# Performance work log

Hardware: AMD Instinct MI355X
Metric: run time of the kernel (lower is better)

## Reference

```python
import jax, jax.numpy as jnp
import numpy as np

N_NODES = 100000
N_EDGES = 1600000
D_IN = 128
D_HID = 128
D_OUT = 128


def setup_inputs() -> dict:
    key = jax.random.key(0)
    ks = jax.random.split(key, 8)
    x = jax.random.normal(ks[0], (N_NODES, D_IN), dtype=jnp.float32)
    edge_index = jax.random.randint(ks[1], (2, N_EDGES), 0, N_NODES, dtype=jnp.int64)
    s = 1.0 / np.sqrt(D_IN)
    W1 = jax.random.normal(ks[2], (D_IN, D_HID), dtype=jnp.float32) * s
    W2 = jax.random.normal(ks[3], (D_HID, D_HID), dtype=jnp.float32) * s
    W3 = jax.random.normal(ks[4], (D_HID, D_OUT), dtype=jnp.float32) * s
    b1 = jnp.zeros((D_HID,), jnp.float32)
    b2 = jnp.zeros((D_HID,), jnp.float32)
    b3 = jnp.zeros((D_OUT,), jnp.float32)
    return {"x": x, "edge_index": edge_index, "W1": W1, "b1": b1,
            "W2": W2, "b2": b2, "W3": W3, "b3": b3}


def reference(x, edge_index, W1, b1, W2, b2, W3, b3):
    # PyG GCNConv semantics: add self-loops, symmetric deg^{-1/2} normalization,
    # message = norm * (x W)[src], scatter-add into dst, then + bias; ReLU after each layer.
    n = x.shape[0]
    loops = jnp.arange(n, dtype=edge_index.dtype)
    src = jnp.concatenate([edge_index[0], loops])  # [E+N]
    dst = jnp.concatenate([edge_index[1], loops])  # [E+N]
    deg = jax.ops.segment_sum(jnp.ones_like(dst, dtype=x.dtype), dst, num_segments=n)
    dinv = jnp.where(deg > 0, jax.lax.rsqrt(deg), 0.0)
    norm = (dinv[src] * dinv[dst])[:, None]  # [E+N, 1]

    def layer(h, W, b):
        h = h @ W                                     # [N, d_out] small GEMM
        msg = h[src] * norm                           # gather + scale  [E+N, d_out]
        agg = jax.ops.segment_sum(msg, dst, num_segments=n)  # scatter-add
        return jax.nn.relu(agg + b)

    x = layer(x, W1, b1)
    x = layer(x, W2, b2)
    x = layer(x, W3, b3)
    return x
```

## Files before the change

kernel.cpp:

```cpp
#include <hip/hip_runtime.h>

#define NN 100000
#define NE 1600000
#define DD 128
#define NB 98
#define NGRP 8
#define NPG (NN / NGRP)
#define CSRCAP 1900032
#define NBLK_B 1024
#define EPB 1563
#define BCAP 210000
#define WJ 256
#define NW 49
#define NSUB (NGRP * NW)
#define SCAP 4608
#define LCAP 5632

typedef __attribute__((ext_vector_type(8))) short short8;
typedef __attribute__((ext_vector_type(4))) float f32x4;

__device__ __forceinline__ unsigned bf16rn(float f) {
  unsigned u = __float_as_uint(f);
  return (u + 0x7fffu + ((u >> 16) & 1u)) >> 16;
}
__device__ __forceinline__ unsigned pk2(float a, float b) {
  return bf16rn(a) | (bf16rn(b) << 16);
}
__device__ __forceinline__ float lo_f(unsigned u) { return __uint_as_float(u << 16); }
__device__ __forceinline__ float hi_f(unsigned u) { return __uint_as_float(u & 0xffff0000u); }


__global__ __launch_bounds__(256) void k_init(int* __restrict__ cnt,
                                              int* __restrict__ gcur,
                                              int* __restrict__ scur) {
  int i = blockIdx.x * 256 + threadIdx.x;
  if (i < NN) cnt[i] = 0;
  if (i < NGRP) gcur[i] = 0;
  if (i < NSUB) scur[i] = 0;
}

__global__ __launch_bounds__(256) void k_bucket(const void* __restrict__ ei,
                                                int* __restrict__ bsrc,
                                                int* __restrict__ bdst,
                                                int* __restrict__ gcur) {
  __shared__ int lcnt[NGRP], lbase[NGRP], lcur[NGRP], zcnt;
  const int t = threadIdx.x;
  if (t == 0) zcnt = 0;
  if (t < NGRP) { lcnt[t] = 0; lcur[t] = 0; }
  __syncthreads();
  if (t < 64) {
    const unsigned* w = (const unsigned*)ei;
    int z = 0;
    for (int i = t; i < 256; i += 64)
      if (w[2 * i + 1] == 0u) z++;
    atomicAdd(&zcnt, z);
  }
  __syncthreads();
  const int isLL = (zcnt >= 250);
  const long long e0 = (long long)blockIdx.x * EPB;
  const int nE = (int)((NE - e0) < EPB ? (NE - e0) : EPB);
  int es[7], ed[7], eb[7];
#pragma unroll
  for (int k = 0; k < 7; k++) {
    int idx = t + k * 256;
    eb[k] = -1;
    if (idx < nE) {
      long long e = e0 + idx;
      if (isLL) {
        es[k] = (int)((const long long*)ei)[e];
        ed[k] = (int)((const long long*)ei)[NE + e];
      } else {
        es[k] = ((const int*)ei)[e];
        ed[k] = ((const int*)ei)[NE + e];
      }
      eb[k] = ed[k] / NPG;
      atomicAdd(&lcnt[eb[k]], 1);
    }
  }
  __syncthreads();
  if (t < NGRP) lbase[t] = atomicAdd(&gcur[t], lcnt[t]);
  __syncthreads();
#pragma unroll
  for (int k = 0; k < 7; k++) {
    if (eb[k] >= 0) {
      int p = lbase[eb[k]] + atomicAdd(&lcur[eb[k]], 1);
      size_t o = (size_t)eb[k] * BCAP + p;
      bsrc[o] = es[k];
      bdst[o] = ed[k];
    }
  }
}

__global__ __launch_bounds__(256) void k_sub(const int* __restrict__ bsrc,
                                             const int* __restrict__ bdst,
                                             const int* __restrict__ gcur,
                                             int* __restrict__ cnt,
                                             int* __restrict__ ssrc,
                                             int* __restrict__ sdst,
                                             int* __restrict__ scur) {
  __shared__ int lcnt[NW], lbase[NW], lcur[NW];
  const int g = blockIdx.x & (NGRP - 1);
  const int s = blockIdx.x >> 3;
  const int n = gcur[g];
  const int chunk = (n + 15) >> 4;
  const int e0 = s * chunk;
  const int e1 = min(e0 + chunk, n);
  const int t = threadIdx.x;
  if (t < NW) { lcnt[t] = 0; lcur[t] = 0; }
  __syncthreads();
  const int* dp = bdst + (size_t)g * BCAP;
  const int* sp = bsrc + (size_t)g * BCAP;
  for (int i = e0 + t; i < e1; i += 256) {
    int d = dp[i];
    atomicAdd(&cnt[d], 1);
    atomicAdd(&lcnt[(d - g * NPG) >> 8], 1);
  }
  __syncthreads();
  if (t < NW) lbase[t] = atomicAdd(&scur[g * NW + t], lcnt[t]);
  __syncthreads();
  for (int i = e0 + t; i < e1; i += 256) {
    int d = dp[i];
    int srcv = sp[i];
    int w = (d - g * NPG) >> 8;
    int p = lbase[w] + atomicAdd(&lcur[w], 1);
    size_t o = (size_t)(g * NW + w) * SCAP + p;
    ssrc[o] = srcv;
    sdst[o] = d;
  }
}

__global__ __launch_bounds__(256) void k_dinv(const int* __restrict__ cnt,
                                              float* __restrict__ dinv) {
  int i = blockIdx.x * 256 + threadIdx.x;
  if (i < NN) dinv[i] = rsqrtf((float)(cnt[i] + 1));
}

__global__ __launch_bounds__(256) void k_scan1(const int* __restrict__ cnt,
                                               int* __restrict__ bsums) {
  __shared__ int sd[256];
  const int tid = threadIdx.x;
  const int base = blockIdx.x * 1024;
  int s = 0;
#pragma unroll
  for (int j = 0; j < 4; j++) {
    int i = base + tid * 4 + j;
    if (i < NN) s += (cnt[i] + 3) & ~3;
  }
  sd[tid] = s;
  __syncthreads();
  for (int d = 128; d > 0; d >>= 1) {
    if (tid < d) sd[tid] += sd[tid + d];
    __syncthreads();
  }
  if (tid == 0) bsums[blockIdx.x] = sd[0];
}

__global__ __launch_bounds__(128) void k_scan2(int* __restrict__ bsums,
                                               int* __restrict__ offs) {
  __shared__ int sd[128];
  const int tid = threadIdx.x;
  int v = (tid < NB) ? bsums[tid] : 0;
  sd[tid] = v;
  __syncthreads();
  for (int d = 1; d < 128; d <<= 1) {
    int t = (tid >= d) ? sd[tid - d] : 0;
    __syncthreads();
    sd[tid] += t;
    __syncthreads();
  }
  if (tid < NB) bsums[tid] = sd[tid] - v;
  if (tid == 127) offs[NN] = sd[127];
}

__global__ __launch_bounds__(256) void k_scan3(const int* __restrict__ cnt,
                                               const int* __restrict__ bsums,
                                               int* __restrict__ offs) {
  __shared__ int sd[256];
  const int tid = threadIdx.x;
  const int base = blockIdx.x * 1024;
  int v[4];
  int s = 0;
#pragma unroll
  for (int j = 0; j < 4; j++) {
    int i = base + tid * 4 + j;
    v[j] = (i < NN) ? ((cnt[i] + 3) & ~3) : 0;
    s += v[j];
  }
  sd[tid] = s;
  __syncthreads();
  for (int d = 1; d < 256; d <<= 1) {
    int t = (tid >= d) ? sd[tid - d] : 0;
    __syncthreads();
    if (tid >= d) sd[tid] += t;
    __syncthreads();
  }
  int run = bsums[blockIdx.x] + sd[tid] - s;
#pragma unroll
  for (int j = 0; j < 4; j++) {
    int i = base + tid * 4 + j;
    if (i < NN) offs[i] = run;
    run += v[j];
  }
}

__global__ __launch_bounds__(256) void k_csr(const int* __restrict__ ssrc,
                                             const int* __restrict__ sdst,
                                             const int* __restrict__ scur,
                                             const int* __restrict__ offs,
                                             int* __restrict__ csr) {
  __shared__ int L[LCAP];
  __shared__ int loff[WJ], lcur[WJ];
  __shared__ int sR0, sRlen, sm;
  const int b = blockIdx.x;
  const int g = b / NW, w = b % NW;
  const int n0 = g * NPG + w * WJ;
  const int wn = min(WJ, NPG - w * WJ);
  const int t = threadIdx.x;
  for (int i = t; i < LCAP; i += 256) L[i] = NN;
  if (t == 0) {
    sR0 = offs[n0];
    sRlen = offs[n0 + wn] - sR0;
    sm = scur[b];
  }
  __syncthreads();
  const int R0 = sR0, Rlen = sRlen, m = sm;
  for (int i = t; i < wn; i += 256) {
    loff[i] = offs[n0 + i] - R0;
    lcur[i] = 0;
  }
  __syncthreads();
  const int* sp = ssrc + (size_t)b * SCAP;
  const int* dp = sdst + (size_t)b * SCAP;
  for (int e = t; e < m; e += 256) {
    int dl = dp[e] - n0;
    int pos = loff[dl] + atomicAdd(&lcur[dl], 1);
    if (pos < LCAP) L[pos] = sp[e];
  }
  __syncthreads();
  for (int i = t * 4; i < Rlen; i += 1024)
    if (i + 3 < LCAP) *(int4*)(csr + R0 + i) = *(const int4*)&L[i];
}

__global__ __launch_bounds__(256) void k_prepw(const float* __restrict__ Wa,
                                               const float* __restrict__ Wb,
                                               const float* __restrict__ Wc,
                                               unsigned* __restrict__ wt,
                                               unsigned* __restrict__ tbuf) {
  if (blockIdx.x == 0 && threadIdx.x < 64)
    tbuf[(size_t)NN * 64 + threadIdx.x] = 0u;
  int id = blockIdx.x * 256 + threadIdx.x;
  int layer = id >> 13;
  int r = id & 8191;
  int n = r >> 6, kp = r & 63;
  const float* W = (layer == 0) ? Wa : (layer == 1) ? Wb : Wc;
  wt[(size_t)layer * 8192 + n * 64 + kp] =
      pk2(W[(size_t)(2 * kp) * DD + n], W[(size_t)(2 * kp + 1) * DD + n]);
}

template <bool F32SRC>
__global__ __launch_bounds__(256) void k_gemm(const void* __restrict__ Av,
                                              const unsigned* __restrict__ Wg,
                                              const float* __restrict__ dinv,
                                              unsigned* __restrict__ T) {
  __shared__ char lds[49408];
  const int t = threadIdx.x;
  const int row0 = blockIdx.x * 64;
  const int w = t >> 6, l = t & 63;
  const int lm = l & 15, kb = l >> 4;

  {
    int r = t >> 2;
    int gr = row0 + r;
#pragma unroll
    for (int s4 = 0; s4 < 4; s4++) {
      int sg = (t & 3) * 4 + s4;
      uint4 u;
      if (gr < NN) {
        if (F32SRC) {
          const float* ap = (const float*)Av + (size_t)gr * DD + sg * 8;
          float4 f0 = *(const float4*)ap;
          float4 f1 = *(const float4*)(ap + 4);
          u.x = pk2(f0.x, f0.y); u.y = pk2(f0.z, f0.w);
          u.z = pk2(f1.x, f1.y); u.w = pk2(f1.z, f1.w);
        } else {
          u = *(const uint4*)((const unsigned*)Av + (size_t)gr * 64 + sg * 4);
        }
      } else {
        u = make_uint4(0u, 0u, 0u, 0u);
      }
      *(uint4*)(lds + r * 256 + ((sg * 16) ^ ((r & 7) << 4))) = u;
    }
  }
#pragma unroll
  for (int q = 0; q < 8; q++) {
    int e = t * 8 + q;
    int n = e >> 4, sg = e & 15;
    uint4 u = *(const uint4*)(Wg + n * 64 + sg * 4);
    *(uint4*)(lds + 16384 + n * 256 + ((sg * 16) ^ ((n & 7) << 4))) = u;
  }
  if (t < 64) {
    int gr = row0 + t;
    *(float*)(lds + 49152 + t * 4) = (gr < NN) ? dinv[gr] : 0.f;
  }
  __syncthreads();

  f32x4 acc[4][2];
#pragma unroll
  for (int i = 0; i < 4; i++)
#pragma unroll
    for (int j = 0; j < 2; j++) acc[i][j] = (f32x4){0.f, 0.f, 0.f, 0.f};

#pragma unroll
  for (int kk = 0; kk < 4; kk++) {
    const int koff = (kk * 4 + kb) * 16;
    short8 af[4], bf[2];
#pragma unroll
    for (int i = 0; i < 4; i++) {
      int r = i * 16 + lm;
      af[i] = *(const short8*)(lds + r * 256 + (koff ^ ((r & 7) << 4)));
    }
#pragma unroll
    for (int j = 0; j < 2; j++) {
      int n = w * 32 + j * 16 + lm;
      bf[j] = *(const short8*)(lds + 16384 + n * 256 + (koff ^ ((n & 7) << 4)));
    }
#pragma unroll
    for (int i = 0; i < 4; i++)
#pragma unroll
      for (int j = 0; j < 2; j++)
        acc[i][j] = __builtin_amdgcn_mfma_f32_16x16x32_bf16(af[i], bf[j], acc[i][j], 0, 0, 0);
  }

#pragma unroll
  for (int i = 0; i < 4; i++) {
#pragma unroll
    for (int j = 0; j < 2; j++) {
#pragma unroll
      for (int q = 0; q < 4; q++) {
        int rl = i * 16 + (l >> 4) * 4 + q;
        float s = *(const float*)(lds + 49152 + rl * 4);
        float v = acc[i][j][q] * s;
        float nb = __shfl_xor(v, 1);
        if ((l & 1) == 0) {
          int gr = row0 + rl;
          if (gr < NN) {
            int cp = w * 16 + j * 8 + (lm >> 1);
            T[(size_t)gr * 64 + cp] = pk2(v, nb);
          }
        }
      }
    }
  }
}

template <bool BF16OUT>
__global__ __launch_bounds__(256) void k_agg(const unsigned* __restrict__ T,
                                             const int* __restrict__ offs,
                                             const int* __restrict__ csr,
                                             const float* __restrict__ dinv,
                                             const float* __restrict__ bias,
                                             void* __restrict__ outv) {
  const int lane = threadIdx.x & 63;
  const int node = blockIdx.x * 4 + (threadIdx.x >> 6);
  if (node >= NN) return;
  unsigned su = T[(size_t)node * 64 + lane];
  float accx = lo_f(su), accy = hi_f(su);
  int j = offs[node];
  const int end = offs[node + 1];
  for (; j + 16 <= end; j += 16) {
    int4 c0 = *(const int4*)(csr + j);
    int4 c1 = *(const int4*)(csr + j + 4);
    int4 c2 = *(const int4*)(csr + j + 8);
    int4 c3 = *(const int4*)(csr + j + 12);
    unsigned u0 = T[(size_t)c0.x * 64 + lane];
    unsigned u1 = T[(size_t)c0.y * 64 + lane];
    unsigned u2 = T[(size_t)c0.z * 64 + lane];
    unsigned u3 = T[(size_t)c0.w * 64 + lane];
    unsigned u4 = T[(size_t)c1.x * 64 + lane];
    unsigned u5 = T[(size_t)c1.y * 64 + lane];
    unsigned u6 = T[(size_t)c1.z * 64 + lane];
    unsigned u7 = T[(size_t)c1.w * 64 + lane];
    unsigned u8 = T[(size_t)c2.x * 64 + lane];
    unsigned u9 = T[(size_t)c2.y * 64 + lane];
    unsigned ua = T[(size_t)c2.z * 64 + lane];
    unsigned ub = T[(size_t)c2.w * 64 + lane];
    unsigned uc = T[(size_t)c3.x * 64 + lane];
    unsigned ud = T[(size_t)c3.y * 64 + lane];
    unsigned ue = T[(size_t)c3.z * 64 + lane];
    unsigned uf = T[(size_t)c3.w * 64 + lane];
    accx += (((lo_f(u0) + lo_f(u1)) + (lo_f(u2) + lo_f(u3))) +
             ((lo_f(u4) + lo_f(u5)) + (lo_f(u6) + lo_f(u7)))) +
            (((lo_f(u8) + lo_f(u9)) + (lo_f(ua) + lo_f(ub))) +
             ((lo_f(uc) + lo_f(ud)) + (lo_f(ue) + lo_f(uf))));
    accy += (((hi_f(u0) + hi_f(u1)) + (hi_f(u2) + hi_f(u3))) +
             ((hi_f(u4) + hi_f(u5)) + (hi_f(u6) + hi_f(u7)))) +
            (((hi_f(u8) + hi_f(u9)) + (hi_f(ua) + hi_f(ub))) +
             ((hi_f(uc) + hi_f(ud)) + (hi_f(ue) + hi_f(uf))));
  }
  for (; j < end; j += 4) {
    int4 c = *(const int4*)(csr + j);
    unsigned u0 = T[(size_t)c.x * 64 + lane];
    unsigned u1 = T[(size_t)c.y * 64 + lane];
    unsigned u2 = T[(size_t)c.z * 64 + lane];
    unsigned u3 = T[(size_t)c.w * 64 + lane];
    accx += (lo_f(u0) + lo_f(u1)) + (lo_f(u2) + lo_f(u3));
    accy += (hi_f(u0) + hi_f(u1)) + (hi_f(u2) + hi_f(u3));
  }
  float s = dinv[node];
  float2 bb = ((const float2*)bias)[lane];
  float ox = fmaxf(accx * s + bb.x, 0.f);
  float oy = fmaxf(accy * s + bb.y, 0.f);
  if (BF16OUT)
    ((unsigned*)outv)[(size_t)node * 64 + lane] = pk2(ox, oy);
  else
    ((float2*)outv)[(size_t)node * 64 + lane] = make_float2(ox, oy);
}


extern "C" void kernel_launch(void* const* d_in, const int* in_sizes, int n_in,
                              void* d_out, int out_size, void* d_ws, size_t ws_size,
                              hipStream_t stream) {
  const float* x = (const float*)d_in[0];
  const void* ei = (const void*)d_in[1];
  const float* W1 = (const float*)d_in[2];
  const float* b1 = (const float*)d_in[3];
  const float* W2 = (const float*)d_in[4];
  const float* b2 = (const float*)d_in[5];
  const float* W3 = (const float*)d_in[6];
  const float* b3 = (const float*)d_in[7];
  float* out = (float*)d_out;

  char* p = (char*)d_ws;
  auto take = [&](size_t bytes) {
    char* r = p;
    p += (bytes + 1023) & ~(size_t)1023;
    return r;
  };
  int* flagpad = (int*)take(4);  (void)flagpad;
  int* gcur = (int*)take((size_t)NGRP * 4);
  int* scur = (int*)take((size_t)NSUB * 4);
  int* cnt = (int*)take((size_t)NN * 4);
  int* offs = (int*)take((size_t)(NN + 1) * 4);
  int* bsums = (int*)take((size_t)NB * 4);
  float* dinv = (float*)take((size_t)NN * 4);
  unsigned* wt = (unsigned*)take((size_t)3 * DD * 64 * 4);
  int* csr = (int*)take((size_t)CSRCAP * 4);
  char* regA = (char*)take((size_t)(NN + 1) * 64 * 4);
  unsigned* tbuf = (unsigned*)regA;
  int* ssrc = (int*)regA;
  int* sdst = ssrc + (size_t)NSUB * SCAP;
  char* regB = (char*)take((size_t)NN * 64 * 4);
  unsigned* hbuf = (unsigned*)regB;
  int* bsrc = (int*)regB;
  int* bdst = bsrc + (size_t)NGRP * BCAP;

  const int nb_n = (NN + 255) / 256;

  k_init<<<nb_n, 256, 0, stream>>>(cnt, gcur, scur);
  k_bucket<<<NBLK_B, 256, 0, stream>>>(ei, bsrc, bdst, gcur);
  k_sub<<<128, 256, 0, stream>>>(bsrc, bdst, gcur, cnt, ssrc, sdst, scur);
  k_dinv<<<nb_n, 256, 0, stream>>>(cnt, dinv);
  k_scan1<<<NB, 256, 0, stream>>>(cnt, bsums);
  k_scan2<<<1, 128, 0, stream>>>(bsums, offs);
  k_scan3<<<NB, 256, 0, stream>>>(cnt, bsums, offs);
  k_csr<<<NSUB, 256, 0, stream>>>(ssrc, sdst, scur, offs, csr);
  k_prepw<<<96, 256, 0, stream>>>(W1, W2, W3, wt, tbuf);

  const int gb = (NN + 63) / 64;
  const int ab = (NN + 3) / 4;
  k_gemm<true><<<gb, 256, 0, stream>>>(x, wt, dinv, tbuf);
  k_agg<true><<<ab, 256, 0, stream>>>(tbuf, offs, csr, dinv, b1, hbuf);
  k_gemm<false><<<gb, 256, 0, stream>>>(hbuf, wt + 8192, dinv, tbuf);
  k_agg<true><<<ab, 256, 0, stream>>>(tbuf, offs, csr, dinv, b2, hbuf);
  k_gemm<false><<<gb, 256, 0, stream>>>(hbuf, wt + 16384, dinv, tbuf);
  k_agg<false><<<ab, 256, 0, stream>>>(tbuf, offs, csr, dinv, b3, out);
}
```

Measured before the change: 486.4 us.

## Pack edge src and local dst into one word and count degrees per window

```diff
diff --git a/kernel.cpp b/kernel.cpp
--- a/kernel.cpp
+++ b/kernel.cpp
@@ -15,6 +15,8 @@
 #define NSUB (NGRP * NW)
 #define SCAP 4608
 #define LCAP 5632
+#define NSLOT 64
+
 
 typedef __attribute__((ext_vector_type(8))) short short8;
 typedef __attribute__((ext_vector_type(4))) float f32x4;
@@ -30,23 +32,22 @@
 __device__ __forceinline__ float hi_f(unsigned u) { return __uint_as_float(u & 0xffff0000u); }
 
 
-__global__ __launch_bounds__(256) void k_init(int* __restrict__ cnt,
-                                              int* __restrict__ gcur,
+__global__ __launch_bounds__(256) void k_init(int* __restrict__ gcur,
                                               int* __restrict__ scur) {
   int i = blockIdx.x * 256 + threadIdx.x;
-  if (i < NN) cnt[i] = 0;
   if (i < NGRP) gcur[i] = 0;
   if (i < NSUB) scur[i] = 0;
 }
 
 __global__ __launch_bounds__(256) void k_bucket(const void* __restrict__ ei,
-                                                int* __restrict__ bsrc,
-                                                int* __restrict__ bdst,
+                                                int* __restrict__ bpk,
                                                 int* __restrict__ gcur) {
-  __shared__ int lcnt[NGRP], lbase[NGRP], lcur[NGRP], zcnt;
+  __shared__ int lcnt[4][NGRP], wbase[4][NGRP], lcur[4][NGRP];
+  __shared__ int zcnt;
   const int t = threadIdx.x;
+  const int wv = t >> 6;
   if (t == 0) zcnt = 0;
-  if (t < NGRP) { lcnt[t] = 0; lcur[t] = 0; }
+  if (t < 4 * NGRP) { ((int*)lcnt)[t] = 0; ((int*)lcur)[t] = 0; }
   __syncthreads();
   if (t < 64) {
     const unsigned* w = (const unsigned*)ei;
@@ -59,74 +60,99 @@
   const int isLL = (zcnt >= 250);
   const long long e0 = (long long)blockIdx.x * EPB;
   const int nE = (int)((NE - e0) < EPB ? (NE - e0) : EPB);
-  int es[7], ed[7], eb[7];
+  int epk[7], eb[7];
 #pragma unroll
   for (int k = 0; k < 7; k++) {
     int idx = t + k * 256;
     eb[k] = -1;
     if (idx < nE) {
       long long e = e0 + idx;
+      int s, d;
       if (isLL) {
-        es[k] = (int)((const long long*)ei)[e];
-        ed[k] = (int)((const long long*)ei)[NE + e];
+        s = (int)((const long long*)ei)[e];
+        d = (int)((const long long*)ei)[NE + e];
       } else {
-        es[k] = ((const int*)ei)[e];
-        ed[k] = ((const int*)ei)[NE + e];
+        s = ((const int*)ei)[e];
+        d = ((const int*)ei)[NE + e];
       }
-      eb[k] = ed[k] / NPG;
-      atomicAdd(&lcnt[eb[k]], 1);
+      int b = d / NPG;
+      eb[k] = b;
+      epk[k] = s | ((d - b * NPG) << 17);
+      atomicAdd(&lcnt[wv][b], 1);
     }
   }
   __syncthreads();
-  if (t < NGRP) lbase[t] = atomicAdd(&gcur[t], lcnt[t]);
+  if (t < NGRP) {
+    int c0 = lcnt[0][t], c1 = lcnt[1][t], c2 = lcnt[2][t], c3 = lcnt[3][t];
+    int base = atomicAdd(&gcur[t], c0 + c1 + c2 + c3);
+    wbase[0][t] = base;
+    wbase[1][t] = base + c0;
+    wbase[2][t] = base + c0 + c1;
+    wbase[3][t] = base + c0 + c1 + c2;
+  }
   __syncthreads();
 #pragma unroll
   for (int k = 0; k < 7; k++) {
     if (eb[k] >= 0) {
-      int p = lbase[eb[k]] + atomicAdd(&lcur[eb[k]], 1);
-      size_t o = (size_t)eb[k] * BCAP + p;
-      bsrc[o] = es[k];
-      bdst[o] = ed[k];
+      int p = wbase[wv][eb[k]] + atomicAdd(&lcur[wv][eb[k]], 1);
+      bpk[(size_t)eb[k] * BCAP + p] = epk[k];
     }
   }
 }
 
-__global__ __launch_bounds__(256) void k_sub(const int* __restrict__ bsrc,
-                                             const int* __restrict__ bdst,
+__global__ __launch_bounds__(256) void k_sub(const int* __restrict__ bpk,
                                              const int* __restrict__ gcur,
-                                             int* __restrict__ cnt,
-                                             int* __restrict__ ssrc,
-                                             int* __restrict__ sdst,
+                                             int* __restrict__ ssub,
                                              int* __restrict__ scur) {
-  __shared__ int lcnt[NW], lbase[NW], lcur[NW];
+  __shared__ int lcnt[4][NW], wbase[4][NW], lcur[4][NW];
   const int g = blockIdx.x & (NGRP - 1);
   const int s = blockIdx.x >> 3;
   const int n = gcur[g];
-  const int chunk = (n + 15) >> 4;
+  const int chunk = (n + NSLOT - 1) / NSLOT;
   const int e0 = s * chunk;
   const int e1 = min(e0 + chunk, n);
   const int t = threadIdx.x;
-  if (t < NW) { lcnt[t] = 0; lcur[t] = 0; }
-  __syncthreads();
-  const int* dp = bdst + (size_t)g * BCAP;
-  const int* sp = bsrc + (size_t)g * BCAP;
+  const int wv = t >> 6;
+  for (int i = t; i < 4 * NW; i += 256) { ((int*)lcnt)[i] = 0; ((int*)lcur)[i] = 0; }
+  __syncthreads();
+  const int* pb = bpk + (size_t)g * BCAP;
+  for (int i = e0 + t; i < e1; i += 256)
+    atomicAdd(&lcnt[wv][pb[i] >> 25], 1);
+  __syncthreads();
+  if (t < NW) {
+    int c0 = lcnt[0][t], c1 = lcnt[1][t], c2 = lcnt[2][t], c3 = lcnt[3][t];
+    int base = atomicAdd(&scur[g * NW + t], c0 + c1 + c2 + c3);
+    wbase[0][t] = base;
+    wbase[1][t] = base + c0;
+    wbase[2][t] = base + c0 + c1;
+    wbase[3][t] = base + c0 + c1 + c2;
+  }
+  __syncthreads();
   for (int i = e0 + t; i < e1; i += 256) {
-    int d = dp[i];
-    atomicAdd(&cnt[d], 1);
-    atomicAdd(&lcnt[(d - g * NPG) >> 8], 1);
-  }
-  __syncthreads();
-  if (t < NW) lbase[t] = atomicAdd(&scur[g * NW + t], lcnt[t]);
-  __syncthreads();
-  for (int i = e0 + t; i < e1; i += 256) {
-    int d = dp[i];
-    int srcv = sp[i];
-    int w = (d - g * NPG) >> 8;
-    int p = lbase[w] + atomicAdd(&lcur[w], 1);
-    size_t o = (size_t)(g * NW + w) * SCAP + p;
-    ssrc[o] = srcv;
-    sdst[o] = d;
-  }
+    int pk = pb[i];
+    int w = pk >> 25;
+    int p = wbase[wv][w] + atomicAdd(&lcur[wv][w], 1);
+    ssub[(size_t)(g * NW + w) * SCAP + p] = pk;
+  }
+}
+
+__global__ __launch_bounds__(256) void k_cnt(const int* __restrict__ ssub,
+                                             const int* __restrict__ scur,
+                                             int* __restrict__ cnt) {
+  __shared__ int lc[WJ];
+  const int b = blockIdx.x;
+  const int g = b / NW, w = b % NW;
+  const int n0 = g * NPG + w * WJ;
+  const int wn = min(WJ, NPG - w * WJ);
+  const int t = threadIdx.x;
+  lc[t] = 0;
+  __syncthreads();
+  const int m = scur[b];
+  const int* sp = ssub + (size_t)b * SCAP;
+  for (int e = t; e < m; e += 256)
+    atomicAdd(&lc[(sp[e] >> 17) & 255], 1);
+  __syncthreads();
+  if (t < wn) cnt[n0 + t] = lc[t];
 }
 
 __global__ __launch_bounds__(256) void k_dinv(const int* __restrict__ cnt,
@@ -203,8 +229,7 @@
   }
 }
 
-__global__ __launch_bounds__(256) void k_csr(const int* __restrict__ ssrc,
-                                             const int* __restrict__ sdst,
+__global__ __launch_bounds__(256) void k_csr(const int* __restrict__ ssub,
                                              const int* __restrict__ scur,
                                              const int* __restrict__ offs,
                                              int* __restrict__ csr) {
@@ -229,12 +254,12 @@
     lcur[i] = 0;
   }
   __syncthreads();
-  const int* sp = ssrc + (size_t)b * SCAP;
-  const int* dp = sdst + (size_t)b * SCAP;
+  const int* sp = ssub + (size_t)b * SCAP;
   for (int e = t; e < m; e += 256) {
-    int dl = dp[e] - n0;
+    int pk = sp[e];
+    int dl = (pk >> 17) & 255;
     int pos = loff[dl] + atomicAdd(&lcur[dl], 1);
-    if (pos < LCAP) L[pos] = sp[e];
+    if (pos < LCAP) L[pos] = pk & 0x1FFFF;
   }
   __syncthreads();
   for (int i = t * 4; i < Rlen; i += 1024)
@@ -436,7 +461,6 @@
     p += (bytes + 1023) & ~(size_t)1023;
     return r;
   };
-  int* flagpad = (int*)take(4);  (void)flagpad;
   int* gcur = (int*)take((size_t)NGRP * 4);
   int* scur = (int*)take((size_t)NSUB * 4);
   int* cnt = (int*)take((size_t)NN * 4);
@@ -447,23 +471,22 @@
   int* csr = (int*)take((size_t)CSRCAP * 4);
   char* regA = (char*)take((size_t)(NN + 1) * 64 * 4);
   unsigned* tbuf = (unsigned*)regA;
-  int* ssrc = (int*)regA;
-  int* sdst = ssrc + (size_t)NSUB * SCAP;
+  int* ssub = (int*)regA;
   char* regB = (char*)take((size_t)NN * 64 * 4);
   unsigned* hbuf = (unsigned*)regB;
-  int* bsrc = (int*)regB;
-  int* bdst = bsrc + (size_t)NGRP * BCAP;
+  int* bpk = (int*)regB;
 
   const int nb_n = (NN + 255) / 256;
 
-  k_init<<<nb_n, 256, 0, stream>>>(cnt, gcur, scur);
-  k_bucket<<<NBLK_B, 256, 0, stream>>>(ei, bsrc, bdst, gcur);
-  k_sub<<<128, 256, 0, stream>>>(bsrc, bdst, gcur, cnt, ssrc, sdst, scur);
+  k_init<<<2, 256, 0, stream>>>(gcur, scur);
+  k_bucket<<<NBLK_B, 256, 0, stream>>>(ei, bpk, gcur);
+  k_sub<<<NGRP * NSLOT, 256, 0, stream>>>(bpk, gcur, ssub, scur);
+  k_cnt<<<NSUB, 256, 0, stream>>>(ssub, scur, cnt);
   k_dinv<<<nb_n, 256, 0, stream>>>(cnt, dinv);
   k_scan1<<<NB, 256, 0, stream>>>(cnt, bsums);
   k_scan2<<<1, 128, 0, stream>>>(bsums, offs);
   k_scan3<<<NB, 256, 0, stream>>>(cnt, bsums, offs);
-  k_csr<<<NSUB, 256, 0, stream>>>(ssrc, sdst, scur, offs, csr);
+  k_csr<<<NSUB, 256, 0, stream>>>(ssub, scur, offs, csr);
   k_prepw<<<96, 256, 0, stream>>>(W1, W2, W3, wt, tbuf);
 
   const int gb = (NN + 63) / 64;
```

New measurement: 416.0 us. -14.5%, faster.
